# Optimization experiments

Measured on AMD Instinct MI355X. Metric: run time of the kernel, lower is better.

## Reference

```python
import jax, jax.numpy as jnp
import numpy as np

B, L, HID, NH = 2, 1024, 1024, 16
HEAD = HID // NH
BUCKETS = 256          # position_buckets -> pos_ebd_size = 256
MAX_POS = 512          # max_relative_positions
ATT_SPAN = BUCKETS     # att_span = pos_ebd_size
SCALE_FACTOR = 3       # 1 + c2p + p2c
EPS = 1e-7


def make_log_bucket_position(rel_pos, bucket_size, max_position):
    sign = jnp.sign(rel_pos)
    mid = bucket_size // 2
    abs_pos = jnp.where((rel_pos < mid) & (rel_pos > -mid), mid - 1, jnp.abs(rel_pos))
    log_pos = jnp.ceil(
        jnp.log(abs_pos.astype(jnp.float32) / mid)
        / np.float32(np.log((max_position - 1) / mid)) * (mid - 1)
    ) + mid
    return jnp.where(abs_pos <= mid, rel_pos.astype(jnp.float32),
                     log_pos * sign.astype(jnp.float32)).astype(jnp.int32)


def build_relative_position(q, k, bucket_size, max_position):
    rel = jnp.arange(q, dtype=jnp.int32)[:, None] - jnp.arange(k, dtype=jnp.int32)[None, :]
    rel = make_log_bucket_position(rel, bucket_size, max_position)
    return rel  # [q, k], values in [-att_span, att_span]


def setup_inputs() -> dict:
    key = jax.random.key(0)
    ks = jax.random.split(key, 12)
    s = 0.02
    return {
        "hidden_states": jax.random.normal(ks[0], (B, L, HID), jnp.float32),
        "attention_mask": jnp.ones((B, 1, L, L), jnp.int32),
        "rel_embeddings": jax.random.normal(ks[1], (2 * ATT_SPAN, HID), jnp.float32),
        "Wq": jax.random.normal(ks[2], (HID, HID), jnp.float32) * s,
        "bq": jnp.zeros((HID,), jnp.float32),
        "Wk": jax.random.normal(ks[3], (HID, HID), jnp.float32) * s,
        "bk": jnp.zeros((HID,), jnp.float32),
        "Wv": jax.random.normal(ks[4], (HID, HID), jnp.float32) * s,
        "bv": jnp.zeros((HID,), jnp.float32),
        "Wo": jax.random.normal(ks[5], (HID, HID), jnp.float32) * s,
        "bo": jnp.zeros((HID,), jnp.float32),
        "ln_gamma": jnp.ones((HID,), jnp.float32),
        "ln_beta": jnp.zeros((HID,), jnp.float32),
    }


def _heads(x):
    # [B, L, HID] -> [B, NH, L, HEAD]
    return x.reshape(x.shape[0], x.shape[1], NH, HEAD).transpose(0, 2, 1, 3)


def reference(hidden_states, attention_mask, rel_embeddings,
              Wq, bq, Wk, bk, Wv, bv, Wo, bo, ln_gamma, ln_beta):
    q = _heads(hidden_states @ Wq + bq)   # [B,NH,L,HEAD]
    k = _heads(hidden_states @ Wk + bk)
    v = _heads(hidden_states @ Wv + bv)

    scale = jnp.sqrt(jnp.float32(HEAD * SCALE_FACTOR))
    scores = jnp.einsum("bhqd,bhkd->bhqk", q, k) / scale  # [B,NH,L,L]

    # ---- disentangled attention bias (share_att_key=True) ----
    rel_pos = build_relative_position(L, L, BUCKETS, MAX_POS)  # [L,L]
    # pos projections reuse query/key projections (share_att_key)
    pos_key = (rel_embeddings @ Wk + bk).reshape(2 * ATT_SPAN, NH, HEAD).transpose(1, 0, 2)   # [NH,2S,HEAD]
    pos_query = (rel_embeddings @ Wq + bq).reshape(2 * ATT_SPAN, NH, HEAD).transpose(1, 0, 2)

    # c2p: content-to-position
    c2p_att = jnp.einsum("bhqd,hsd->bhqs", q, pos_key)                 # [B,NH,L,2S]
    c2p_pos = jnp.clip(rel_pos + ATT_SPAN, 0, 2 * ATT_SPAN - 1)        # [L,L]
    c2p_idx = jnp.broadcast_to(c2p_pos[None, None], (B, NH, L, L))
    c2p = jnp.take_along_axis(c2p_att, c2p_idx, axis=-1)               # [B,NH,L,L]

    # p2c: position-to-content
    p2c_att = jnp.einsum("bhkd,hsd->bhks", k, pos_query)               # [B,NH,L,2S]
    p2c_pos = jnp.clip(-rel_pos + ATT_SPAN, 0, 2 * ATT_SPAN - 1)       # [L,L]
    p2c_idx = jnp.broadcast_to(p2c_pos[None, None], (B, NH, L, L))
    p2c = jnp.take_along_axis(p2c_att, p2c_idx, axis=-1)               # [B,NH,K,Q]
    p2c = p2c.transpose(0, 1, 3, 2)                                    # [B,NH,Q,K]

    scores = scores + (c2p + p2c) / scale

    # ---- XSoftmax: masked softmax ----
    rmask = attention_mask == 0  # [B,1,L,L] broadcasts over heads
    logits = jnp.where(rmask, -jnp.inf, scores)
    probs = jax.nn.softmax(logits, axis=-1)
    probs = jnp.where(rmask, 0.0, probs)

    ctx = jnp.einsum("bhqk,bhkd->bhqd", probs, v)                      # [B,NH,L,HEAD]
    ctx = ctx.transpose(0, 2, 1, 3).reshape(B, L, HID)

    # ---- SelfOutput: dense + residual + LayerNorm ----
    out = ctx @ Wo + bo
    x = out + hidden_states
    mu = jnp.mean(x, axis=-1, keepdims=True)
    var = jnp.mean(jnp.square(x - mu), axis=-1, keepdims=True)
    return (x - mu) / jnp.sqrt(var + EPS) * ln_gamma + ln_beta
```

## Files before the change

kernel.cpp:

```cpp
#include <hip/hip_runtime.h>
#include <hip/hip_bf16.h>
#include <cstdint>
#include <cstddef>

typedef float f32x4 __attribute__((ext_vector_type(4)));
typedef short s16x8 __attribute__((ext_vector_type(8)));

#define OFF_IDX   0ull
#define OFF_XB    4096ull
#define OFF_WT    5246976ull
#define OFF_Q     13635584ull
#define OFF_K     17829888ull
#define OFF_VT    22024192ull
#define OFF_POSQ  26218496ull
#define OFF_POSK  27267072ull
#define OFF_C2P   28315648ull
#define OFF_P2C   61870080ull
#define OFF_CTX   95424512ull
#define OFF_X     99618816ull

#define INV_SCALE 0.07216878364870322f

__device__ __forceinline__ short f2bf(float f) {
  unsigned u = __builtin_bit_cast(unsigned, f);
  unsigned r = (u + 0x7fffu + ((u >> 16) & 1u)) >> 16;
  return (short)r;
}
__device__ __forceinline__ float bf2f(short h) {
  unsigned u = ((unsigned)(unsigned short)h) << 16;
  return __builtin_bit_cast(float, u);
}

__global__ void build_idx(char* wsb) {
  int i = blockIdx.x * 256 + threadIdx.x;
  if (i >= 2047) return;
  int d = i - 1023;
  int ad = d < 0 ? -d : d;
  int bucket;
  if (ad <= 128) {
    bucket = d;
  } else {
    const float denom = 1.38433933f;
    float lp = ceilf(logf((float)ad * (1.0f / 128.0f)) / denom * 127.0f) + 128.0f;
    bucket = (int)lp * (d > 0 ? 1 : -1);
  }
  int idx = bucket + 256;
  idx = idx < 0 ? 0 : (idx > 511 ? 511 : idx);
  ((short*)(wsb + OFF_IDX))[i] = (short)idx;
}

__global__ __launch_bounds__(256) void convert_x(const float* __restrict__ hidden,
                                                 const float* __restrict__ rel,
                                                 char* __restrict__ wsb) {
  size_t gid = (size_t)blockIdx.x * 256 + threadIdx.x;
  const float* src = (gid < 524288) ? (hidden + gid * 4) : (rel + (gid - 524288) * 4);
  float4 v = *(const float4*)src;
  short* dst = (short*)(wsb + OFF_XB) + gid * 4;
  short4 o;
  o.x = f2bf(v.x); o.y = f2bf(v.y); o.z = f2bf(v.z); o.w = f2bf(v.w);
  *(short4*)dst = o;
}

__global__ __launch_bounds__(256) void transpose_w(const float* __restrict__ Wq,
                                                   const float* __restrict__ Wk,
                                                   const float* __restrict__ Wv,
                                                   const float* __restrict__ Wo,
                                                   char* __restrict__ wsb) {
  int z = blockIdx.z;
  const float* W = (z == 0) ? Wq : (z == 1) ? Wk : (z == 2) ? Wv : Wo;
  short* out = (short*)(wsb + OFF_WT) + (size_t)z * 1048576;
  int n0 = blockIdx.x * 32, k0 = blockIdx.y * 32;
  int tx = threadIdx.x & 31, ty = threadIdx.x >> 5;
  __shared__ float t[32][33];
#pragma unroll
  for (int i = 0; i < 4; ++i)
    t[ty + 8 * i][tx] = W[(size_t)(k0 + ty + 8 * i) * 1024 + n0 + tx];
  __syncthreads();
#pragma unroll
  for (int i = 0; i < 4; ++i)
    out[(size_t)(n0 + ty + 8 * i) * 1024 + k0 + tx] = f2bf(t[tx][ty + 8 * i]);
}

__global__ __launch_bounds__(256) void gemm_all(char* __restrict__ wsb, int mode,
    const float* __restrict__ bq, const float* __restrict__ bk, const float* __restrict__ bv,
    const float* __restrict__ bo, const float* __restrict__ hidden) {
  const int tid = threadIdx.x;
  const int w = tid >> 6, l = tid & 63;
  const int lr = l & 15, lg = l >> 4;
  const int wr = (w >> 1) * 64, wc = (w & 1) * 64;
  const int n0 = blockIdx.x * 128, m0 = blockIdx.y * 128;
  const int z = blockIdx.z;

  const short* A;
  const short* B;
  int lda, ldb, K;
  if (mode == 0) {
    if (z == 2 && m0 >= 2048) return;
    A = (const short*)(wsb + OFF_XB); lda = 1024;
    B = (const short*)(wsb + OFF_WT) + (size_t)z * 1048576; ldb = 1024;
    K = 1024;
  } else if (mode == 1) {
    int which = z >> 5, bh = z & 31, h = bh & 15;
    A = (const short*)(wsb + (which ? OFF_K : OFF_Q)) + (size_t)bh * 65536; lda = 64;
    B = (const short*)(wsb + (which ? OFF_POSQ : OFF_POSK)) + (size_t)h * 32768; ldb = 64;
    K = 64;
  } else {
    A = (const short*)(wsb + OFF_CTX); lda = 1024;
    B = (const short*)(wsb + OFF_WT) + (size_t)3 * 1048576; ldb = 1024;
    K = 1024;
  }

  __shared__ __align__(16) short Al[128 * 32];
  __shared__ __align__(16) short Bl[128 * 32];

  f32x4 acc[4][4] = {};

  for (int k0 = 0; k0 < K; k0 += 32) {
#pragma unroll
    for (int j = 0; j < 2; ++j) {
      int c = w * 2 + j;
      int row = c * 16 + (l >> 2), col = (l & 3) * 8;
      const short* ga = A + (size_t)(m0 + row) * lda + k0 + col;
      const short* gb = B + (size_t)(n0 + row) * ldb + k0 + col;
      __builtin_amdgcn_global_load_lds((const __attribute__((address_space(1))) void*)ga,
          (__attribute__((address_space(3))) void*)(Al + c * 512), 16, 0, 0);
      __builtin_amdgcn_global_load_lds((const __attribute__((address_space(1))) void*)gb,
          (__attribute__((address_space(3))) void*)(Bl + c * 512), 16, 0, 0);
    }
    __syncthreads();
    s16x8 af[4], bfr[4];
#pragma unroll
    for (int i = 0; i < 4; ++i) af[i] = *(const s16x8*)&Al[(wr + i * 16 + lr) * 32 + lg * 8];
#pragma unroll
    for (int i = 0; i < 4; ++i) bfr[i] = *(const s16x8*)&Bl[(wc + i * 16 + lr) * 32 + lg * 8];
#pragma unroll
    for (int mi = 0; mi < 4; ++mi)
#pragma unroll
      for (int ni = 0; ni < 4; ++ni)
        acc[mi][ni] = __builtin_amdgcn_mfma_f32_16x16x32_bf16(af[mi], bfr[ni], acc[mi][ni], 0, 0, 0);
    __syncthreads();
  }

  if (mode == 0) {
    const float* bias = (z == 0) ? bq : (z == 1) ? bk : bv;
    short* outq = (short*)(wsb + ((z == 0) ? OFF_Q : (z == 1) ? OFF_K : OFF_VT));
    short* outp = (short*)(wsb + ((z == 0) ? OFF_POSQ : OFF_POSK));
#pragma unroll
    for (int mi = 0; mi < 4; ++mi) {
#pragma unroll
      for (int ni = 0; ni < 4; ++ni) {
        int gcol = n0 + wc + ni * 16 + lr;
        int h = gcol >> 6, d = gcol & 63;
        float bia = bias[gcol];
#pragma unroll
        for (int r = 0; r < 4; ++r) {
          int grow = m0 + wr + mi * 16 + lg * 4 + r;
          short v16 = f2bf(acc[mi][ni][r] + bia);
          if (z == 2) {
            int b = grow >> 10, ll = grow & 1023;
            outq[((size_t)((b * 16 + h) * 64 + d)) * 1024 + ll] = v16;
          } else if (grow < 2048) {
            int b = grow >> 10, ll = grow & 1023;
            outq[((size_t)((b * 16 + h) * 1024 + ll)) * 64 + d] = v16;
          } else {
            int s = grow - 2048;
            outp[((size_t)(h * 512 + s)) * 64 + d] = v16;
          }
        }
      }
    }
  } else if (mode == 1) {
    int which = z >> 5, bh = z & 31;
    short* C = (short*)(wsb + (which ? OFF_P2C : OFF_C2P)) + (size_t)bh * 524288;
#pragma unroll
    for (int mi = 0; mi < 4; ++mi)
#pragma unroll
      for (int ni = 0; ni < 4; ++ni)
#pragma unroll
        for (int r = 0; r < 4; ++r) {
          int grow = m0 + wr + mi * 16 + lg * 4 + r;
          int gcol = n0 + wc + ni * 16 + lr;
          C[(size_t)grow * 512 + gcol] = f2bf(acc[mi][ni][r]);
        }
  } else {
    float* X = (float*)(wsb + OFF_X);
#pragma unroll
    for (int mi = 0; mi < 4; ++mi)
#pragma unroll
      for (int ni = 0; ni < 4; ++ni) {
        int gcol = n0 + wc + ni * 16 + lr;
        float bia = bo[gcol];
#pragma unroll
        for (int r = 0; r < 4; ++r) {
          int grow = m0 + wr + mi * 16 + lg * 4 + r;
          X[(size_t)grow * 1024 + gcol] =
              acc[mi][ni][r] + bia + hidden[(size_t)grow * 1024 + gcol];
        }
      }
  }
}

__global__ __launch_bounds__(256) void attn_kernel(char* __restrict__ wsb,
                                                   const int* __restrict__ mask) {
  const int bh = blockIdx.x, qt = blockIdx.y;
  const int b = bh >> 4, h = bh & 15;
  const int q0 = qt * 64;
  const int tid = threadIdx.x, w = tid >> 6, l = tid & 63;
  const int lr = l & 15, lg = l >> 4;

  const short* qb  = (const short*)(wsb + OFF_Q)  + (size_t)bh * 65536;
  const short* kb  = (const short*)(wsb + OFF_K)  + (size_t)bh * 65536;
  const short* vtb = (const short*)(wsb + OFF_VT) + (size_t)bh * 65536;
  const short* c2pb = (const short*)(wsb + OFF_C2P) + (size_t)bh * 524288;
  const short* p2cb = (const short*)(wsb + OFF_P2C) + (size_t)bh * 524288;
  const short* idxg = (const short*)(wsb + OFF_IDX);

  __shared__ __align__(16) short Kl[64][88];
  __shared__ __align__(16) short Vl[64][88];
  __shared__ __align__(16) short Pl[4][16][88];
  __shared__ __align__(16) short c2ps[64][128];
  __shared__ __align__(16) short p2cs[64][128];
  __shared__ short idxt[2048];

  for (int i = tid; i < 2047; i += 256) idxt[i] = idxg[i];

  s16x8 qf0, qf1;
  {
    int g = q0 + w * 16 + lr;
    const short* qp = qb + (size_t)g * 64 + lg * 8;
    qf0 = *(const s16x8*)qp;
    qf1 = *(const s16x8*)(qp + 32);
  }

  f32x4 acc[4] = {};
  float mrun[4] = {-1e30f, -1e30f, -1e30f, -1e30f};
  float lsum[4] = {0.f, 0.f, 0.f, 0.f};
  __syncthreads();

  for (int kt = 0; kt < 16; ++kt) {
    const int k0 = kt * 64;
    {
      int row = tid >> 2, c0 = (tid & 3) * 16;
      const short* ks = kb + (size_t)(k0 + row) * 64 + c0;
      *(s16x8*)&Kl[row][c0]     = *(const s16x8*)ks;
      *(s16x8*)&Kl[row][c0 + 8] = *(const s16x8*)(ks + 8);
      const short* vs = vtb + (size_t)row * 1024 + k0 + c0;
      *(s16x8*)&Vl[row][c0]     = *(const s16x8*)vs;
      *(s16x8*)&Vl[row][c0 + 8] = *(const s16x8*)(vs + 8);
    }
    const int lo = idxt[(q0 - k0 - 63) + 1023];
    {
      int row = tid >> 2, j0 = (tid & 3) * 32;
      const short* cs = c2pb + (size_t)(q0 + row) * 512;
      const short* ps = p2cb + (size_t)(k0 + row) * 512;
#pragma unroll
      for (int g2 = 0; g2 < 4; ++g2) {
        int j = j0 + g2 * 8;
        int sc = lo + j;
        if (sc + 7 <= 511) {
          *(s16x8*)&c2ps[row][j] = *(const s16x8*)(cs + sc);
          *(s16x8*)&p2cs[row][j] = *(const s16x8*)(ps + sc);
        } else {
          for (int i2 = 0; i2 < 8; ++i2) {
            int scc = sc + i2; scc = scc > 511 ? 511 : scc;
            c2ps[row][j + i2] = cs[scc];
            p2cs[row][j + i2] = ps[scc];
          }
        }
      }
    }
    __syncthreads();

    f32x4 sf[4];
#pragma unroll
    for (int cb = 0; cb < 4; ++cb) {
      s16x8 kf0 = *(const s16x8*)&Kl[cb * 16 + lr][lg * 8];
      s16x8 kf1 = *(const s16x8*)&Kl[cb * 16 + lr][32 + lg * 8];
      f32x4 z4 = {};
      z4 = __builtin_amdgcn_mfma_f32_16x16x32_bf16(qf0, kf0, z4, 0, 0, 0);
      z4 = __builtin_amdgcn_mfma_f32_16x16x32_bf16(qf1, kf1, z4, 0, 0, 0);
      sf[cb] = z4;
    }

    float pv[4][4];
    float tmax[4] = {-1e30f, -1e30f, -1e30f, -1e30f};
#pragma unroll
    for (int cb = 0; cb < 4; ++cb) {
      int colt = cb * 16 + lr;
      int gk = k0 + colt;
#pragma unroll
      for (int r = 0; r < 4; ++r) {
        int rowt = w * 16 + lg * 4 + r;
        int gq = q0 + rowt;
        int wl = idxt[(gq - gk) + 1023] - lo;
        float bias = bf2f(c2ps[rowt][wl]) + bf2f(p2cs[colt][wl]);
        float sv = (sf[cb][r] + bias) * INV_SCALE;
        int mv = mask[((size_t)b * 1024 + gq) * 1024 + gk];
        sv = mv ? sv : -1e30f;
        pv[cb][r] = sv;
        tmax[r] = fmaxf(tmax[r], sv);
      }
    }
#pragma unroll
    for (int off = 1; off < 16; off <<= 1)
#pragma unroll
      for (int r = 0; r < 4; ++r) tmax[r] = fmaxf(tmax[r], __shfl_xor(tmax[r], off));
    float alpha[4];
#pragma unroll
    for (int r = 0; r < 4; ++r) {
      float mn = fmaxf(mrun[r], tmax[r]);
      alpha[r] = __expf(mrun[r] - mn);
      mrun[r] = mn;
    }
    float rsum[4] = {0.f, 0.f, 0.f, 0.f};
#pragma unroll
    for (int cb = 0; cb < 4; ++cb)
#pragma unroll
      for (int r = 0; r < 4; ++r) {
        float p = __expf(pv[cb][r] - mrun[r]);
        pv[cb][r] = p;
        rsum[r] += p;
      }
#pragma unroll
    for (int off = 1; off < 16; off <<= 1)
#pragma unroll
      for (int r = 0; r < 4; ++r) rsum[r] += __shfl_xor(rsum[r], off);
#pragma unroll
    for (int r = 0; r < 4; ++r) lsum[r] = lsum[r] * alpha[r] + rsum[r];
#pragma unroll
    for (int d2 = 0; d2 < 4; ++d2)
#pragma unroll
      for (int r = 0; r < 4; ++r) acc[d2][r] *= alpha[r];

#pragma unroll
    for (int cb = 0; cb < 4; ++cb)
#pragma unroll
      for (int r = 0; r < 4; ++r)
        Pl[w][lg * 4 + r][cb * 16 + lr] = f2bf(pv[cb][r]);

    s16x8 pa0 = *(const s16x8*)&Pl[w][lr][lg * 8];
    s16x8 pa1 = *(const s16x8*)&Pl[w][lr][32 + lg * 8];
#pragma unroll
    for (int d2 = 0; d2 < 4; ++d2) {
      s16x8 vf0 = *(const s16x8*)&Vl[d2 * 16 + lr][lg * 8];
      s16x8 vf1 = *(const s16x8*)&Vl[d2 * 16 + lr][32 + lg * 8];
      acc[d2] = __builtin_amdgcn_mfma_f32_16x16x32_bf16(pa0, vf0, acc[d2], 0, 0, 0);
      acc[d2] = __builtin_amdgcn_mfma_f32_16x16x32_bf16(pa1, vf1, acc[d2], 0, 0, 0);
    }
    __syncthreads();
  }

  short* ctx = (short*)(wsb + OFF_CTX);
#pragma unroll
  for (int r = 0; r < 4; ++r) {
    float inv = 1.0f / lsum[r];
    int gq = q0 + w * 16 + lg * 4 + r;
#pragma unroll
    for (int d2 = 0; d2 < 4; ++d2) {
      int gd = h * 64 + d2 * 16 + lr;
      ctx[((size_t)b * 1024 + gq) * 1024 + gd] = f2bf(acc[d2][r] * inv);
    }
  }
}

__global__ __launch_bounds__(256) void ln_kernel(const char* __restrict__ wsb,
                                                 const float* __restrict__ gamma,
                                                 const float* __restrict__ beta,
                                                 float* __restrict__ out) {
  int row = blockIdx.x, tid = threadIdx.x;
  const float* x = (const float*)(wsb + OFF_X) + (size_t)row * 1024;
  float4 v = ((const float4*)x)[tid];
  float s = v.x + v.y + v.z + v.w;
  float s2 = v.x * v.x + v.y * v.y + v.z * v.z + v.w * v.w;
#pragma unroll
  for (int off = 1; off < 64; off <<= 1) {
    s += __shfl_xor(s, off);
    s2 += __shfl_xor(s2, off);
  }
  __shared__ float ss[4], ss2[4];
  if ((tid & 63) == 0) { ss[tid >> 6] = s; ss2[tid >> 6] = s2; }
  __syncthreads();
  s = ss[0] + ss[1] + ss[2] + ss[3];
  s2 = ss2[0] + ss2[1] + ss2[2] + ss2[3];
  float mu = s * (1.0f / 1024.0f);
  float var = s2 * (1.0f / 1024.0f) - mu * mu;
  float rstd = rsqrtf(var + 1e-7f);
  float4 g = ((const float4*)gamma)[tid];
  float4 be = ((const float4*)beta)[tid];
  float4 o;
  o.x = (v.x - mu) * rstd * g.x + be.x;
  o.y = (v.y - mu) * rstd * g.y + be.y;
  o.z = (v.z - mu) * rstd * g.z + be.z;
  o.w = (v.w - mu) * rstd * g.w + be.w;
  ((float4*)(out + (size_t)row * 1024))[tid] = o;
}

extern "C" void kernel_launch(void* const* d_in, const int* in_sizes, int n_in,
                              void* d_out, int out_size, void* d_ws, size_t ws_size,
                              hipStream_t stream) {
  const float* hidden = (const float*)d_in[0];
  const int*   mask   = (const int*)d_in[1];
  const float* rel    = (const float*)d_in[2];
  const float* Wq = (const float*)d_in[3];
  const float* bq = (const float*)d_in[4];
  const float* Wk = (const float*)d_in[5];
  const float* bk = (const float*)d_in[6];
  const float* Wv = (const float*)d_in[7];
  const float* bv = (const float*)d_in[8];
  const float* Wo = (const float*)d_in[9];
  const float* bo = (const float*)d_in[10];
  const float* gamma = (const float*)d_in[11];
  const float* beta  = (const float*)d_in[12];
  char* ws = (char*)d_ws;
  float* out = (float*)d_out;

  build_idx<<<dim3(8), dim3(256), 0, stream>>>(ws);
  convert_x<<<dim3(2560), dim3(256), 0, stream>>>(hidden, rel, ws);
  transpose_w<<<dim3(32, 32, 4), dim3(256), 0, stream>>>(Wq, Wk, Wv, Wo, ws);
  gemm_all<<<dim3(8, 20, 3), dim3(256), 0, stream>>>(ws, 0, bq, bk, bv, bo, hidden);
  gemm_all<<<dim3(4, 8, 64), dim3(256), 0, stream>>>(ws, 1, bq, bk, bv, bo, hidden);
  attn_kernel<<<dim3(32, 16), dim3(256), 0, stream>>>(ws, mask);
  gemm_all<<<dim3(8, 16, 1), dim3(256), 0, stream>>>(ws, 2, bq, bk, bv, bo, hidden);
  ln_kernel<<<dim3(2048), dim3(256), 0, stream>>>(ws, gamma, beta, out);
}
```

Before: 336.5 us.

## Fuse c2p/p2c position GEMMs into attention and pack mask into bitwords

Removes the separate mode-1 GEMM that wrote full c2p/p2c tables (about 64 MB of bf16 per call) to global memory. The attention kernel now computes only the needed window of each per-tile position score with MFMA against the position embeddings. The int32 mask is packed into 64-bit ballot words by a new pre-kernel, and K/V shared tiles use an XOR swizzle instead of padding. In exchange there is redundant MFMA work per tile, an extra barrier, and an added launch_bounds occupancy hint.

```diff
diff --git a/kernel.cpp b/kernel.cpp
--- a/kernel.cpp
+++ b/kernel.cpp
@@ -14,8 +14,7 @@
 #define OFF_VT    22024192ull
 #define OFF_POSQ  26218496ull
 #define OFF_POSK  27267072ull
-#define OFF_C2P   28315648ull
-#define OFF_P2C   61870080ull
+#define OFF_MB    28315648ull
 #define OFF_CTX   95424512ull
 #define OFF_X     99618816ull
 
@@ -49,6 +48,16 @@
   ((short*)(wsb + OFF_IDX))[i] = (short)idx;
 }
 
+__global__ __launch_bounds__(256) void build_maskbits(const int* __restrict__ mask,
+                                                      char* __restrict__ wsb) {
+  int word = blockIdx.x * 4 + (threadIdx.x >> 6);
+  int lane = threadIdx.x & 63;
+  int q = word & 1023, kt = (word >> 10) & 15, b = word >> 14;
+  int mv = mask[((size_t)b * 1024 + q) * 1024 + kt * 64 + lane];
+  unsigned long long bits = __ballot(mv != 0);
+  if (lane == 0) ((unsigned long long*)(wsb + OFF_MB))[word] = bits;
+}
+
 __global__ __launch_bounds__(256) void convert_x(const float* __restrict__ hidden,
                                                  const float* __restrict__ rel,
                                                  char* __restrict__ wsb) {
@@ -99,11 +108,6 @@
     A = (const short*)(wsb + OFF_XB); lda = 1024;
     B = (const short*)(wsb + OFF_WT) + (size_t)z * 1048576; ldb = 1024;
     K = 1024;
-  } else if (mode == 1) {
-    int which = z >> 5, bh = z & 31, h = bh & 15;
-    A = (const short*)(wsb + (which ? OFF_K : OFF_Q)) + (size_t)bh * 65536; lda = 64;
-    B = (const short*)(wsb + (which ? OFF_POSQ : OFF_POSK)) + (size_t)h * 32768; ldb = 64;
-    K = 64;
   } else {
     A = (const short*)(wsb + OFF_CTX); lda = 1024;
     B = (const short*)(wsb + OFF_WT) + (size_t)3 * 1048576; ldb = 1024;
@@ -169,19 +173,6 @@
         }
       }
     }
-  } else if (mode == 1) {
-    int which = z >> 5, bh = z & 31;
-    short* C = (short*)(wsb + (which ? OFF_P2C : OFF_C2P)) + (size_t)bh * 524288;
-#pragma unroll
-    for (int mi = 0; mi < 4; ++mi)
-#pragma unroll
-      for (int ni = 0; ni < 4; ++ni)
-#pragma unroll
-        for (int r = 0; r < 4; ++r) {
-          int grow = m0 + wr + mi * 16 + lg * 4 + r;
-          int gcol = n0 + wc + ni * 16 + lr;
-          C[(size_t)grow * 512 + gcol] = f2bf(acc[mi][ni][r]);
-        }
   } else {
     float* X = (float*)(wsb + OFF_X);
 #pragma unroll
@@ -200,8 +191,7 @@
   }
 }
 
-__global__ __launch_bounds__(256) void attn_kernel(char* __restrict__ wsb,
-                                                   const int* __restrict__ mask) {
+__global__ __launch_bounds__(256, 3) void attn_kernel(char* __restrict__ wsb) {
   const int bh = blockIdx.x, qt = blockIdx.y;
   const int b = bh >> 4, h = bh & 15;
   const int q0 = qt * 64;
@@ -211,18 +201,19 @@
   const short* qb  = (const short*)(wsb + OFF_Q)  + (size_t)bh * 65536;
   const short* kb  = (const short*)(wsb + OFF_K)  + (size_t)bh * 65536;
   const short* vtb = (const short*)(wsb + OFF_VT) + (size_t)bh * 65536;
-  const short* c2pb = (const short*)(wsb + OFF_C2P) + (size_t)bh * 524288;
-  const short* p2cb = (const short*)(wsb + OFF_P2C) + (size_t)bh * 524288;
+  const short* pkb = (const short*)(wsb + OFF_POSK) + (size_t)h * 32768;
+  const short* pqb = (const short*)(wsb + OFF_POSQ) + (size_t)h * 32768;
   const short* idxg = (const short*)(wsb + OFF_IDX);
-
-  __shared__ __align__(16) short Kl[64][88];
-  __shared__ __align__(16) short Vl[64][88];
-  __shared__ __align__(16) short Pl[4][16][88];
-  __shared__ __align__(16) short c2ps[64][128];
-  __shared__ __align__(16) short p2cs[64][128];
-  __shared__ short idxt[2048];
-
-  for (int i = tid; i < 2047; i += 256) idxt[i] = idxg[i];
+  const unsigned long long* mb =
+      (const unsigned long long*)(wsb + OFF_MB) + (size_t)b * 16384;
+
+  __shared__ __align__(16) short Kl[4096];
+  __shared__ __align__(16) short Vl[4096];
+  __shared__ __align__(16) short c2pw[4][16][104];
+  __shared__ __align__(16) short p2cw[64][104];
+  __shared__ __align__(16) short iiall[1088];
+
+  for (int j = tid; j < 1087; j += 256) iiall[j] = idxg[q0 + j];
 
   s16x8 qf0, qf1;
   {
@@ -240,63 +231,93 @@
   for (int kt = 0; kt < 16; ++kt) {
     const int k0 = kt * 64;
     {
-      int row = tid >> 2, c0 = (tid & 3) * 16;
-      const short* ks = kb + (size_t)(k0 + row) * 64 + c0;
-      *(s16x8*)&Kl[row][c0]     = *(const s16x8*)ks;
-      *(s16x8*)&Kl[row][c0 + 8] = *(const s16x8*)(ks + 8);
-      const short* vs = vtb + (size_t)row * 1024 + k0 + c0;
-      *(s16x8*)&Vl[row][c0]     = *(const s16x8*)vs;
-      *(s16x8*)&Vl[row][c0 + 8] = *(const s16x8*)(vs + 8);
-    }
-    const int lo = idxt[(q0 - k0 - 63) + 1023];
+      int srow = tid >> 2, sc2 = (tid & 3) * 2, rx = srow & 7;
+      const short* ks = kb + (size_t)(k0 + srow) * 64 + sc2 * 8;
+      *(s16x8*)&Kl[srow * 64 + ((sc2 ^ rx) << 3)]       = *(const s16x8*)ks;
+      *(s16x8*)&Kl[srow * 64 + (((sc2 + 1) ^ rx) << 3)] = *(const s16x8*)(ks + 8);
+      const short* vs = vtb + (size_t)srow * 1024 + k0 + sc2 * 8;
+      *(s16x8*)&Vl[srow * 64 + ((sc2 ^ rx) << 3)]       = *(const s16x8*)vs;
+      *(s16x8*)&Vl[srow * 64 + (((sc2 + 1) ^ rx) << 3)] = *(const s16x8*)(vs + 8);
+    }
+    unsigned long long mw[4];
+#pragma unroll
+    for (int r = 0; r < 4; ++r)
+      mw[r] = mb[(size_t)kt * 1024 + q0 + w * 16 + lg * 4 + r];
+    __syncthreads();
+
+    const int jbase = 960 - k0;
+    const int loC  = iiall[w * 16 + jbase] & ~7;
+    const int loPw = iiall[48 - w * 16 + jbase] & ~7;
+    int loP[4];
+#pragma unroll
+    for (int cb = 0; cb < 4; ++cb) loP[cb] = iiall[48 - cb * 16 + jbase] & ~7;
+
     {
-      int row = tid >> 2, j0 = (tid & 3) * 32;
-      const short* cs = c2pb + (size_t)(q0 + row) * 512;
-      const short* ps = p2cb + (size_t)(k0 + row) * 512;
-#pragma unroll
-      for (int g2 = 0; g2 < 4; ++g2) {
-        int j = j0 + g2 * 8;
-        int sc = lo + j;
-        if (sc + 7 <= 511) {
-          *(s16x8*)&c2ps[row][j] = *(const s16x8*)(cs + sc);
-          *(s16x8*)&p2cs[row][j] = *(const s16x8*)(ps + sc);
-        } else {
-          for (int i2 = 0; i2 < 8; ++i2) {
-            int scc = sc + i2; scc = scc > 511 ? 511 : scc;
-            c2ps[row][j + i2] = cs[scc];
-            p2cs[row][j + i2] = ps[scc];
-          }
-        }
-      }
-    }
-    __syncthreads();
-
+      f32x4 cacc[6] = {};
+#pragma unroll
+      for (int cb = 0; cb < 6; ++cb) {
+        int i0 = loC + cb * 16 + lr;
+        i0 = i0 > 511 ? 511 : i0;
+        const short* bp = pkb + (size_t)i0 * 64 + lg * 8;
+        s16x8 b0 = *(const s16x8*)bp;
+        s16x8 b1 = *(const s16x8*)(bp + 32);
+        cacc[cb] = __builtin_amdgcn_mfma_f32_16x16x32_bf16(qf0, b0, cacc[cb], 0, 0, 0);
+        cacc[cb] = __builtin_amdgcn_mfma_f32_16x16x32_bf16(qf1, b1, cacc[cb], 0, 0, 0);
+      }
+#pragma unroll
+      for (int cb = 0; cb < 6; ++cb)
+#pragma unroll
+        for (int r = 0; r < 4; ++r)
+          c2pw[w][lg * 4 + r][cb * 16 + lr] = f2bf(cacc[cb][r]);
+    }
+    {
+      int krow = w * 16 + lr, rx = krow & 7;
+      s16x8 ka0 = *(const s16x8*)&Kl[krow * 64 + ((lg ^ rx) << 3)];
+      s16x8 ka1 = *(const s16x8*)&Kl[krow * 64 + (((4 + lg) ^ rx) << 3)];
+      f32x4 pacc[6] = {};
+#pragma unroll
+      for (int cb = 0; cb < 6; ++cb) {
+        int i0 = loPw + cb * 16 + lr;
+        i0 = i0 > 511 ? 511 : i0;
+        const short* bp = pqb + (size_t)i0 * 64 + lg * 8;
+        s16x8 b0 = *(const s16x8*)bp;
+        s16x8 b1 = *(const s16x8*)(bp + 32);
+        pacc[cb] = __builtin_amdgcn_mfma_f32_16x16x32_bf16(ka0, b0, pacc[cb], 0, 0, 0);
+        pacc[cb] = __builtin_amdgcn_mfma_f32_16x16x32_bf16(ka1, b1, pacc[cb], 0, 0, 0);
+      }
+#pragma unroll
+      for (int cb = 0; cb < 6; ++cb)
+#pragma unroll
+        for (int r = 0; r < 4; ++r)
+          p2cw[w * 16 + lg * 4 + r][cb * 16 + lr] = f2bf(pacc[cb][r]);
+    }
     f32x4 sf[4];
 #pragma unroll
     for (int cb = 0; cb < 4; ++cb) {
-      s16x8 kf0 = *(const s16x8*)&Kl[cb * 16 + lr][lg * 8];
-      s16x8 kf1 = *(const s16x8*)&Kl[cb * 16 + lr][32 + lg * 8];
+      int krow = cb * 16 + lr, rx = krow & 7;
+      s16x8 kf0 = *(const s16x8*)&Kl[krow * 64 + ((lg ^ rx) << 3)];
+      s16x8 kf1 = *(const s16x8*)&Kl[krow * 64 + (((4 + lg) ^ rx) << 3)];
       f32x4 z4 = {};
       z4 = __builtin_amdgcn_mfma_f32_16x16x32_bf16(qf0, kf0, z4, 0, 0, 0);
       z4 = __builtin_amdgcn_mfma_f32_16x16x32_bf16(qf1, kf1, z4, 0, 0, 0);
       sf[cb] = z4;
     }
+    __syncthreads();
 
     float pv[4][4];
     float tmax[4] = {-1e30f, -1e30f, -1e30f, -1e30f};
 #pragma unroll
     for (int cb = 0; cb < 4; ++cb) {
       int colt = cb * 16 + lr;
-      int gk = k0 + colt;
 #pragma unroll
       for (int r = 0; r < 4; ++r) {
-        int rowt = w * 16 + lg * 4 + r;
-        int gq = q0 + rowt;
-        int wl = idxt[(gq - gk) + 1023] - lo;
-        float bias = bf2f(c2ps[rowt][wl]) + bf2f(p2cs[colt][wl]);
+        int rowl = lg * 4 + r;
+        int jj = (w * 16 + rowl) - colt + 1023 - k0;
+        int i = iiall[jj];
+        float bias = bf2f(c2pw[w][rowl][i - loC]) + bf2f(p2cw[colt][i - loP[cb]]);
         float sv = (sf[cb][r] + bias) * INV_SCALE;
-        int mv = mask[((size_t)b * 1024 + gq) * 1024 + gk];
-        sv = mv ? sv : -1e30f;
+        bool ok = (mw[r] >> colt) & 1ull;
+        sv = ok ? sv : -1e30f;
         pv[cb][r] = sv;
         tmax[r] = fmaxf(tmax[r], sv);
       }
@@ -336,14 +357,15 @@
     for (int cb = 0; cb < 4; ++cb)
 #pragma unroll
       for (int r = 0; r < 4; ++r)
-        Pl[w][lg * 4 + r][cb * 16 + lr] = f2bf(pv[cb][r]);
-
-    s16x8 pa0 = *(const s16x8*)&Pl[w][lr][lg * 8];
-    s16x8 pa1 = *(const s16x8*)&Pl[w][lr][32 + lg * 8];
+        c2pw[w][lg * 4 + r][cb * 16 + lr] = f2bf(pv[cb][r]);
+
+    s16x8 pa0 = *(const s16x8*)&c2pw[w][lr][lg * 8];
+    s16x8 pa1 = *(const s16x8*)&c2pw[w][lr][32 + lg * 8];
 #pragma unroll
     for (int d2 = 0; d2 < 4; ++d2) {
-      s16x8 vf0 = *(const s16x8*)&Vl[d2 * 16 + lr][lg * 8];
-      s16x8 vf1 = *(const s16x8*)&Vl[d2 * 16 + lr][32 + lg * 8];
+      int drow = d2 * 16 + lr, rx = drow & 7;
+      s16x8 vf0 = *(const s16x8*)&Vl[drow * 64 + ((lg ^ rx) << 3)];
+      s16x8 vf1 = *(const s16x8*)&Vl[drow * 64 + (((4 + lg) ^ rx) << 3)];
       acc[d2] = __builtin_amdgcn_mfma_f32_16x16x32_bf16(pa0, vf0, acc[d2], 0, 0, 0);
       acc[d2] = __builtin_amdgcn_mfma_f32_16x16x32_bf16(pa1, vf1, acc[d2], 0, 0, 0);
     }
@@ -415,11 +437,11 @@
   float* out = (float*)d_out;
 
   build_idx<<<dim3(8), dim3(256), 0, stream>>>(ws);
+  build_maskbits<<<dim3(8192), dim3(256), 0, stream>>>(mask, ws);
   convert_x<<<dim3(2560), dim3(256), 0, stream>>>(hidden, rel, ws);
   transpose_w<<<dim3(32, 32, 4), dim3(256), 0, stream>>>(Wq, Wk, Wv, Wo, ws);
   gemm_all<<<dim3(8, 20, 3), dim3(256), 0, stream>>>(ws, 0, bq, bk, bv, bo, hidden);
-  gemm_all<<<dim3(4, 8, 64), dim3(256), 0, stream>>>(ws, 1, bq, bk, bv, bo, hidden);
-  attn_kernel<<<dim3(32, 16), dim3(256), 0, stream>>>(ws, mask);
+  attn_kernel<<<dim3(32, 16), dim3(256), 0, stream>>>(ws);
   gemm_all<<<dim3(8, 16, 1), dim3(256), 0, stream>>>(ws, 2, bq, bk, bv, bo, hidden);
   ln_kernel<<<dim3(2048), dim3(256), 0, stream>>>(ws, gamma, beta, out);
 }
```

Result: faster. 298.8 us (-11.2%).
